# Optimization experiments

Hardware: AMD Instinct MI355X
Metric: run time of the kernel (lower is better)

## Reference

```python
import jax, jax.numpy as jnp
import numpy as np

D = 640
I = 640
K = 4  # experts per token
E = 32
T = 64
EPS = 1e-5
LIMIT = 7.0


def setup_inputs() -> dict:
    key = jax.random.key(0)
    ks = jax.random.split(key, 8)
    return {
        "x": jax.random.normal(ks[0], (1, D, 1, T), dtype=jnp.float32),
        "norm_w": jax.random.uniform(ks[1], (D,), dtype=jnp.float32) + 0.5,
        "gate_w": jax.random.normal(ks[2], (E, D), dtype=jnp.float32) * 0.05,
        "gate_b": jax.random.normal(ks[3], (E,), dtype=jnp.float32) * 0.05,
        "w1": jax.random.normal(ks[4], (E, D, 2 * I), dtype=jnp.float32) * 0.02,
        "b1": jax.random.normal(ks[5], (E, 2 * I), dtype=jnp.float32) * 0.02,
        "w2": jax.random.normal(ks[6], (E, I, D), dtype=jnp.float32) * 0.02,
        "b2": jax.random.normal(ks[7], (E, D), dtype=jnp.float32) * 0.02,
    }


def reference(x, norm_w, gate_w, gate_b, w1, b1, w2, b2):
    residual = x
    # RMSNorm over channel dim (axis=1) of (1, D, 1, T)
    var = jnp.mean(x * x, axis=1, keepdims=True)
    normed = x * jax.lax.rsqrt(var + EPS) * norm_w.reshape(-1, 1, 1)
    # (1, D, 1, T) -> (T, D)
    t = normed[0, :, 0, :].T
    # router
    g = t @ gate_w.T + gate_b                       # (T, E)
    top_vals, top_idx = jax.lax.top_k(g, K)        # (T, K)
    ew = jax.nn.softmax(top_vals, axis=-1)          # (T, K)
    # gather per-token expert weights (faithful to index_select pattern)
    w1s = w1[top_idx]                               # (T, K, D, 2I)
    b1s = b1[top_idx]                               # (T, K, 2I)
    h = jnp.einsum('td,tkdi->tki', t, w1s) + b1s    # (T, K, 2I)
    h_glu = jnp.minimum(h[..., :I], LIMIT)
    h_lin = jnp.clip(h[..., I:], -LIMIT, LIMIT)
    h_act = h_glu * jax.nn.sigmoid(1.702 * h_glu) * (h_lin + 1.0)  # (T, K, I)
    out = jnp.einsum('tki,tkid->tkd', h_act, w2[top_idx]) + b2[top_idx]  # (T, K, D)
    out = jnp.sum(out * ew[..., None], axis=1)      # (T, D)
    out = out.T[None, :, None, :]                   # (1, D, 1, T)
    return residual + out
```

## Files before the change

### kernel.cpp

```cpp
#include <hip/hip_runtime.h>
#include <math.h>

#define DDIM 640
#define IDIM 640
#define TWO_I 1280
#define KSEL 4
#define NEXP 32
#define NTOK 64
#define NPAIR 256
#define EPSV 1e-5f
#define LIMIT 7.0f
#define CHUNK 16
#define RC 8
#define RLEN 80

#define WAITVM(n) asm volatile("s_waitcnt vmcnt(" #n ")" ::: "memory")
#define RAWBAR() __builtin_amdgcn_s_barrier()
#define GLL(gp, lp)                                                            \
    __builtin_amdgcn_global_load_lds(                                          \
        (const __attribute__((address_space(1))) void*)(gp),                   \
        (__attribute__((address_space(3))) void*)(lp), 16, 0, 0)


__global__ void k_rmsnorm(const float* __restrict__ x, const float* __restrict__ nw,
                          float* __restrict__ tws, int* __restrict__ counts) {
    const int t = blockIdx.x;
    const int tid = threadIdx.x;
    if (blockIdx.x == 0 && tid < NEXP) counts[tid] = 0;
    __shared__ float red[256];
    float s = 0.f;
    for (int d = tid; d < DDIM; d += 256) {
        float v = x[d * NTOK + t];
        s += v * v;
    }
    red[tid] = s;
    __syncthreads();
    for (int off = 128; off > 0; off >>= 1) {
        if (tid < off) red[tid] += red[tid + off];
        __syncthreads();
    }
    const float rs = 1.0f / sqrtf(red[0] * (1.0f / DDIM) + EPSV);
    for (int d = tid; d < DDIM; d += 256) {
        tws[t * DDIM + d] = x[d * NTOK + t] * rs * nw[d];
    }
}

__global__ void k_router(const float* __restrict__ tws, const float* __restrict__ gw,
                         const float* __restrict__ gb, float* __restrict__ ew,
                         int* __restrict__ counts, int* __restrict__ list,
                         int* __restrict__ pexp) {
    const int t = blockIdx.x;
    const int lane = threadIdx.x;
    __shared__ float lg[NEXP];
    if (lane < NEXP) {
        const float* g = gw + lane * DDIM;
        const float* tr = tws + t * DDIM;
        float acc = 0.f;
        for (int d = 0; d < DDIM; d += 4) {
            acc = fmaf(tr[d], g[d], acc);
            acc = fmaf(tr[d + 1], g[d + 1], acc);
            acc = fmaf(tr[d + 2], g[d + 2], acc);
            acc = fmaf(tr[d + 3], g[d + 3], acc);
        }
        lg[lane] = acc + gb[lane];
    }
    __syncthreads();
    if (lane == 0) {
        float vals[KSEL];
        int idx[KSEL];
        for (int k = 0; k < KSEL; ++k) {
            float best = -1e30f;
            int bi = 0;
            for (int e = 0; e < NEXP; ++e) {
                float v = lg[e];
                if (v > best) { best = v; bi = e; }
            }
            vals[k] = best;
            idx[k] = bi;
            lg[bi] = -1e30f;
        }
        const float m = vals[0];
        float ex[KSEL];
        float se = 0.f;
        for (int k = 0; k < KSEL; ++k) { ex[k] = __expf(vals[k] - m); se += ex[k]; }
        const float inv = 1.0f / se;
        for (int k = 0; k < KSEL; ++k) {
            const int p = t * KSEL + k;
            ew[p] = ex[k] * inv;
            pexp[p] = idx[k];
            const int slot = atomicAdd(&counts[idx[k]], 1);
            list[idx[k] * NTOK + slot] = p;
        }
    }
}

__global__ __launch_bounds__(320, 1) void k_ffn1(const float* __restrict__ tws,
                                                 const float* __restrict__ w1,
                                                 float* __restrict__ hpart,
                                                 const int* __restrict__ counts,
                                                 const int* __restrict__ list) {
    const int rc = blockIdx.x;
    const int e = blockIdx.y;
    const int cnt = counts[e];
    const int tid = threadIdx.x;
    const int wid = tid >> 6;
    const int lane = tid & 63;
    const int col0 = wid * 256 + lane * 4;
    const int d0 = rc * RLEN;

    __shared__ float wlds[2][8 * TWO_I];
    __shared__ float tl[CHUNK][RLEN];

    const float* wpanel = w1 + (size_t)e * DDIM * TWO_I + (size_t)d0 * TWO_I;

    for (int c0 = 0; c0 < cnt; c0 += CHUNK) {
        int pid[CHUNK];
#pragma unroll
        for (int s = 0; s < CHUNK; ++s) {
            int ii = c0 + s;
            ii = (ii < cnt) ? ii : c0;
            pid[s] = list[e * NTOK + ii];
        }
        __syncthreads();
#pragma unroll
        for (int s = 0; s < CHUNK; ++s)
            for (int d = tid; d < RLEN; d += 320)
                tl[s][d] = tws[(pid[s] >> 2) * DDIM + d0 + d];
        __syncthreads();

        float acc[CHUNK][4];
#pragma unroll
        for (int s = 0; s < CHUNK; ++s)
#pragma unroll
            for (int c = 0; c < 4; ++c) acc[s][c] = 0.f;

#pragma unroll
        for (int k = 0; k < 8; ++k)
            GLL(wpanel + wid * 2048 + k * 256 + lane * 4, &wlds[0][wid * 2048 + k * 256]);

        for (int t = 0; t < 10; ++t) {
            const int cur = t & 1;
            if (t + 1 < 10) {
                const int nxt = (t + 1) & 1;
                const float* gsrc = wpanel + (size_t)(t + 1) * 8 * TWO_I;
#pragma unroll
                for (int k = 0; k < 8; ++k)
                    GLL(gsrc + wid * 2048 + k * 256 + lane * 4, &wlds[nxt][wid * 2048 + k * 256]);
                WAITVM(8);
            } else {
                WAITVM(0);
            }
            RAWBAR();
#pragma unroll
            for (int r = 0; r < 8; ++r) {
                const float4 w = *reinterpret_cast<const float4*>(&wlds[cur][r * TWO_I + col0]);
                const int row = t * 8 + r;
#pragma unroll
                for (int s = 0; s < CHUNK; ++s) {
                    const float tv = tl[s][row];
                    acc[s][0] = fmaf(tv, w.x, acc[s][0]);
                    acc[s][1] = fmaf(tv, w.y, acc[s][1]);
                    acc[s][2] = fmaf(tv, w.z, acc[s][2]);
                    acc[s][3] = fmaf(tv, w.w, acc[s][3]);
                }
            }
            RAWBAR();
        }

#pragma unroll
        for (int s = 0; s < CHUNK; ++s) {
            float4 v = make_float4(acc[s][0], acc[s][1], acc[s][2], acc[s][3]);
            *reinterpret_cast<float4*>(&hpart[((size_t)rc * NPAIR + pid[s]) * TWO_I + col0]) = v;
        }
    }
}

__global__ void k_reduce1(const float* __restrict__ hpart, const float* __restrict__ b1,
                          const int* __restrict__ pexp, float* __restrict__ hact) {
    const int p = blockIdx.x;
    const int e = pexp[p];
    for (int i = threadIdx.x; i < IDIM; i += 256) {
        float g = 0.f, l = 0.f;
#pragma unroll
        for (int rc = 0; rc < RC; ++rc) {
            g += hpart[((size_t)rc * NPAIR + p) * TWO_I + i];
            l += hpart[((size_t)rc * NPAIR + p) * TWO_I + i + IDIM];
        }
        float hg = fminf(g + b1[e * TWO_I + i], LIMIT);
        float hl = l + b1[e * TWO_I + IDIM + i];
        hl = fminf(fmaxf(hl, -LIMIT), LIMIT);
        const float sig = 1.0f / (1.0f + __expf(-1.702f * hg));
        hact[(size_t)p * IDIM + i] = hg * sig * (hl + 1.0f);
    }
}

__global__ __launch_bounds__(320, 1) void k_ffn2(const float* __restrict__ hact,
                                                 const float* __restrict__ w2,
                                                 float* __restrict__ hpart2,
                                                 const int* __restrict__ counts,
                                                 const int* __restrict__ list) {
    const int rc = blockIdx.x;
    const int e = blockIdx.y;
    const int cnt = counts[e];
    const int tid = threadIdx.x;
    const int wid = tid >> 6;
    const int lane = tid & 63;
    const int col0 = tid * 2;
    const int i0 = rc * RLEN;

    __shared__ float wlds[2][16 * DDIM];
    __shared__ float tl[CHUNK][RLEN];

    const float* wpanel = w2 + (size_t)e * IDIM * DDIM + (size_t)i0 * DDIM;

    for (int c0 = 0; c0 < cnt; c0 += CHUNK) {
        int pid[CHUNK];
#pragma unroll
        for (int s = 0; s < CHUNK; ++s) {
            int ii = c0 + s;
            ii = (ii < cnt) ? ii : c0;
            pid[s] = list[e * NTOK + ii];
        }
        __syncthreads();
#pragma unroll
        for (int s = 0; s < CHUNK; ++s)
            for (int d = tid; d < RLEN; d += 320)
                tl[s][d] = hact[(size_t)pid[s] * IDIM + i0 + d];
        __syncthreads();

        float acc[CHUNK][2];
#pragma unroll
        for (int s = 0; s < CHUNK; ++s) { acc[s][0] = 0.f; acc[s][1] = 0.f; }

#pragma unroll
        for (int k = 0; k < 8; ++k)
            GLL(wpanel + wid * 2048 + k * 256 + lane * 4, &wlds[0][wid * 2048 + k * 256]);

        for (int t = 0; t < 5; ++t) {
            const int cur = t & 1;
            if (t + 1 < 5) {
                const int nxt = (t + 1) & 1;
                const float* gsrc = wpanel + (size_t)(t + 1) * 16 * DDIM;
#pragma unroll
                for (int k = 0; k < 8; ++k)
                    GLL(gsrc + wid * 2048 + k * 256 + lane * 4, &wlds[nxt][wid * 2048 + k * 256]);
                WAITVM(8);
            } else {
                WAITVM(0);
            }
            RAWBAR();
#pragma unroll
            for (int r = 0; r < 16; ++r) {
                const float2 w = *reinterpret_cast<const float2*>(&wlds[cur][r * DDIM + col0]);
                const int row = t * 16 + r;
#pragma unroll
                for (int s = 0; s < CHUNK; ++s) {
                    const float hv = tl[s][row];
                    acc[s][0] = fmaf(hv, w.x, acc[s][0]);
                    acc[s][1] = fmaf(hv, w.y, acc[s][1]);
                }
            }
            RAWBAR();
        }

#pragma unroll
        for (int s = 0; s < CHUNK; ++s) {
            float2 v = make_float2(acc[s][0], acc[s][1]);
            *reinterpret_cast<float2*>(&hpart2[((size_t)rc * NPAIR + pid[s]) * DDIM + col0]) = v;
        }
    }
}

__global__ void k_final(const float* __restrict__ x, const float* __restrict__ hpart2,
                        const float* __restrict__ b2, const float* __restrict__ ew,
                        const int* __restrict__ pexp, float* __restrict__ out) {
    const int t = blockIdx.x;
    for (int d = threadIdx.x; d < DDIM; d += 256) {
        float v = x[d * NTOK + t];
#pragma unroll
        for (int k = 0; k < KSEL; ++k) {
            const int p = t * KSEL + k;
            const int e = pexp[p];
            float s = 0.f;
#pragma unroll
            for (int rc = 0; rc < RC; ++rc)
                s += hpart2[((size_t)rc * NPAIR + p) * DDIM + d];
            v += (s + b2[e * DDIM + d]) * ew[p];
        }
        out[d * NTOK + t] = v;
    }
}

extern "C" void kernel_launch(void* const* d_in, const int* in_sizes, int n_in,
                              void* d_out, int out_size, void* d_ws, size_t ws_size,
                              hipStream_t stream) {
    const float* x  = (const float*)d_in[0];
    const float* nw = (const float*)d_in[1];
    const float* gw = (const float*)d_in[2];
    const float* gb = (const float*)d_in[3];
    const float* w1 = (const float*)d_in[4];
    const float* b1 = (const float*)d_in[5];
    const float* w2 = (const float*)d_in[6];
    const float* b2 = (const float*)d_in[7];
    float* out = (float*)d_out;

    float* ws    = (float*)d_ws;
    float* tws   = ws;
    float* hact  = ws + 40960;
    float* hpart = ws + 204800;
    float* ew    = ws + 2826240;
    int* counts  = (int*)(ws + 2826496);
    int* list    = (int*)(ws + 2826528);
    int* pexp    = (int*)(ws + 2828576);

    hipLaunchKernelGGL(k_rmsnorm, dim3(NTOK), dim3(256), 0, stream, x, nw, tws, counts);
    hipLaunchKernelGGL(k_router, dim3(NTOK), dim3(64), 0, stream, tws, gw, gb, ew, counts, list, pexp);
    hipLaunchKernelGGL(k_ffn1, dim3(RC, NEXP), dim3(320), 0, stream, tws, w1, hpart, counts, list);
    hipLaunchKernelGGL(k_reduce1, dim3(NPAIR), dim3(256), 0, stream, hpart, b1, pexp, hact);
    hipLaunchKernelGGL(k_ffn2, dim3(RC, NEXP), dim3(320), 0, stream, hact, w2, hpart, counts, list);
    hipLaunchKernelGGL(k_final, dim3(NTOK), dim3(256), 0, stream, x, hpart, b2, ew, pexp, out);
}
```

Measured before the change: 80.60 us.

## Parallelize router dot products and remap ffn1 LDS reads to float2 strips

The router now uses 256 threads, with 8 threads per expert each computing an 80-element partial dot product through float4 loads. The partials are reduced in shared memory, replacing the serial 32-lane loop over all 640 elements. In ffn1 each thread now reads contiguous float2 pairs across 16 half-rows of the staged weight tile and splits results into gate and linear accumulators, changing the LDS access pattern and the hpart store layout. The per-thread accumulator count stays the same, but LDS reads grow from 8 to 16 per tile, and the new mapping of tile columns to output columns must still be correct.

```diff
diff --git a/kernel.cpp b/kernel.cpp
--- a/kernel.cpp
+++ b/kernel.cpp
@@ -50,30 +50,42 @@
                          int* __restrict__ counts, int* __restrict__ list,
                          int* __restrict__ pexp) {
     const int t = blockIdx.x;
-    const int lane = threadIdx.x;
+    const int tid = threadIdx.x;
+    const int e = tid >> 3;
+    const int sub = tid & 7;
+    __shared__ float part[256];
     __shared__ float lg[NEXP];
-    if (lane < NEXP) {
-        const float* g = gw + lane * DDIM;
-        const float* tr = tws + t * DDIM;
+    {
+        const float* tr = tws + t * DDIM + sub * 80;
+        const float* g = gw + e * DDIM + sub * 80;
         float acc = 0.f;
-        for (int d = 0; d < DDIM; d += 4) {
-            acc = fmaf(tr[d], g[d], acc);
-            acc = fmaf(tr[d + 1], g[d + 1], acc);
-            acc = fmaf(tr[d + 2], g[d + 2], acc);
-            acc = fmaf(tr[d + 3], g[d + 3], acc);
-        }
-        lg[lane] = acc + gb[lane];
+#pragma unroll
+        for (int i = 0; i < 20; ++i) {
+            const float4 a = *reinterpret_cast<const float4*>(tr + i * 4);
+            const float4 b = *reinterpret_cast<const float4*>(g + i * 4);
+            acc = fmaf(a.x, b.x, acc);
+            acc = fmaf(a.y, b.y, acc);
+            acc = fmaf(a.z, b.z, acc);
+            acc = fmaf(a.w, b.w, acc);
+        }
+        part[tid] = acc;
     }
     __syncthreads();
-    if (lane == 0) {
+    if (sub == 0) {
+        float s = part[tid] + part[tid + 1] + part[tid + 2] + part[tid + 3] +
+                  part[tid + 4] + part[tid + 5] + part[tid + 6] + part[tid + 7];
+        lg[e] = s + gb[e];
+    }
+    __syncthreads();
+    if (tid == 0) {
         float vals[KSEL];
         int idx[KSEL];
         for (int k = 0; k < KSEL; ++k) {
             float best = -1e30f;
             int bi = 0;
-            for (int e = 0; e < NEXP; ++e) {
-                float v = lg[e];
-                if (v > best) { best = v; bi = e; }
+            for (int x2 = 0; x2 < NEXP; ++x2) {
+                float v = lg[x2];
+                if (v > best) { best = v; bi = x2; }
             }
             vals[k] = best;
             idx[k] = bi;
@@ -105,7 +117,6 @@
     const int tid = threadIdx.x;
     const int wid = tid >> 6;
     const int lane = tid & 63;
-    const int col0 = wid * 256 + lane * 4;
     const int d0 = rc * RLEN;
 
     __shared__ float wlds[2][8 * TWO_I];
@@ -128,11 +139,13 @@
                 tl[s][d] = tws[(pid[s] >> 2) * DDIM + d0 + d];
         __syncthreads();
 
-        float acc[CHUNK][4];
-#pragma unroll
-        for (int s = 0; s < CHUNK; ++s)
-#pragma unroll
-            for (int c = 0; c < 4; ++c) acc[s][c] = 0.f;
+        float accg[CHUNK][2];
+        float accl[CHUNK][2];
+#pragma unroll
+        for (int s = 0; s < CHUNK; ++s) {
+            accg[s][0] = 0.f; accg[s][1] = 0.f;
+            accl[s][0] = 0.f; accl[s][1] = 0.f;
+        }
 
 #pragma unroll
         for (int k = 0; k < 8; ++k)
@@ -141,7 +154,7 @@
         for (int t = 0; t < 10; ++t) {
             const int cur = t & 1;
             if (t + 1 < 10) {
-                const int nxt = (t + 1) & 1;
+                const int nxt = cur ^ 1;
                 const float* gsrc = wpanel + (size_t)(t + 1) * 8 * TWO_I;
 #pragma unroll
                 for (int k = 0; k < 8; ++k)
@@ -152,16 +165,23 @@
             }
             RAWBAR();
 #pragma unroll
-            for (int r = 0; r < 8; ++r) {
-                const float4 w = *reinterpret_cast<const float4*>(&wlds[cur][r * TWO_I + col0]);
-                const int row = t * 8 + r;
-#pragma unroll
-                for (int s = 0; s < CHUNK; ++s) {
-                    const float tv = tl[s][row];
-                    acc[s][0] = fmaf(tv, w.x, acc[s][0]);
-                    acc[s][1] = fmaf(tv, w.y, acc[s][1]);
-                    acc[s][2] = fmaf(tv, w.z, acc[s][2]);
-                    acc[s][3] = fmaf(tv, w.w, acc[s][3]);
+            for (int h = 0; h < 16; ++h) {
+                const float2 w = *reinterpret_cast<const float2*>(&wlds[cur][h * 640 + tid * 2]);
+                const int row = t * 8 + (h >> 1);
+                if ((h & 1) == 0) {
+#pragma unroll
+                    for (int s = 0; s < CHUNK; ++s) {
+                        const float tv = tl[s][row];
+                        accg[s][0] = fmaf(tv, w.x, accg[s][0]);
+                        accg[s][1] = fmaf(tv, w.y, accg[s][1]);
+                    }
+                } else {
+#pragma unroll
+                    for (int s = 0; s < CHUNK; ++s) {
+                        const float tv = tl[s][row];
+                        accl[s][0] = fmaf(tv, w.x, accl[s][0]);
+                        accl[s][1] = fmaf(tv, w.y, accl[s][1]);
+                    }
                 }
             }
             RAWBAR();
@@ -169,8 +189,9 @@
 
 #pragma unroll
         for (int s = 0; s < CHUNK; ++s) {
-            float4 v = make_float4(acc[s][0], acc[s][1], acc[s][2], acc[s][3]);
-            *reinterpret_cast<float4*>(&hpart[((size_t)rc * NPAIR + pid[s]) * TWO_I + col0]) = v;
+            float* dst = &hpart[((size_t)rc * NPAIR + pid[s]) * TWO_I];
+            *reinterpret_cast<float2*>(dst + tid * 2) = make_float2(accg[s][0], accg[s][1]);
+            *reinterpret_cast<float2*>(dst + IDIM + tid * 2) = make_float2(accl[s][0], accl[s][1]);
         }
     }
 }
@@ -239,7 +260,7 @@
         for (int t = 0; t < 5; ++t) {
             const int cur = t & 1;
             if (t + 1 < 5) {
-                const int nxt = (t + 1) & 1;
+                const int nxt = cur ^ 1;
                 const float* gsrc = wpanel + (size_t)(t + 1) * 16 * DDIM;
 #pragma unroll
                 for (int k = 0; k < 8; ++k)
@@ -314,7 +335,7 @@
     int* pexp    = (int*)(ws + 2828576);
 
     hipLaunchKernelGGL(k_rmsnorm, dim3(NTOK), dim3(256), 0, stream, x, nw, tws, counts);
-    hipLaunchKernelGGL(k_router, dim3(NTOK), dim3(64), 0, stream, tws, gw, gb, ew, counts, list, pexp);
+    hipLaunchKernelGGL(k_router, dim3(NTOK), dim3(256), 0, stream, tws, gw, gb, ew, counts, list, pexp);
     hipLaunchKernelGGL(k_ffn1, dim3(RC, NEXP), dim3(320), 0, stream, tws, w1, hpart, counts, list);
     hipLaunchKernelGGL(k_reduce1, dim3(NPAIR), dim3(256), 0, stream, hpart, b1, pexp, hact);
     hipLaunchKernelGGL(k_ffn2, dim3(RC, NEXP), dim3(320), 0, stream, hact, w2, hpart, counts, list);
```

Result: slower. 85.49 us (+6.1%).
